# Kernel tuning notes

Hardware: AMD Instinct MI355X
Metric: run time of the kernel (lower is better)

Reference implementation:

```python
import jax, jax.numpy as jnp
import numpy as np

MOMENTUM = 0.99
EPS = 1e-5


def setup_inputs() -> dict:
    key = jax.random.key(0)
    k1, k2, k3, k4 = jax.random.split(key, 4)
    x = jax.random.normal(k1, (16, 256, 64, 64), dtype=jnp.float32)
    embed = jax.random.normal(k2, (2048, 256), dtype=jnp.float32)
    cluster_size = jax.random.uniform(k3, (2048,), dtype=jnp.float32)
    embed_avg = jax.random.normal(k4, (256, 2048), dtype=jnp.float32)
    return {"x": x, "embed": embed, "cluster_size": cluster_size, "embed_avg": embed_avg}


def reference(x, embed, cluster_size, embed_avg):
    # x: (b, c, h, w) with c == emb_dim; embed: (D, c)
    b, c, h, w = x.shape
    D = embed.shape[0]
    # flatten exactly as the torch code: transpose(1,-1) then reshape(-1, c)
    flat = jnp.swapaxes(x, 1, 3).reshape(-1, c)  # (N, c), N = b*w*h
    # L2 kNN with k=1, expressed as argmax of 2*q.k - |k|^2 - |q|^2 (as in _torch_knn)
    scores = (2.0 * (flat @ embed.T)
              - jnp.sum(embed * embed, axis=1)[None, :]
              - jnp.sum(flat * flat, axis=1, keepdims=True))  # (N, D)
    ids_flat = jnp.argmax(scores, axis=1)  # (N,)
    ids = ids_flat.reshape(b, h, w)
    # lookup + transpose(1,-1), mirroring the original op sequence
    quantized = jnp.swapaxes(embed[ids], 1, 3)  # (b, c, w, h) == (b, c, h, w) since h == w
    commit_loss = jnp.mean((x - quantized) ** 2)
    # EMA statistics (training branch). one-hot matmul expressed as segment sums (same math).
    onehot_sum = jax.ops.segment_sum(jnp.ones_like(ids_flat, dtype=flat.dtype), ids_flat,
                                     num_segments=D)  # (D,)
    embed_sum = jax.ops.segment_sum(flat, ids_flat, num_segments=D).T  # (c, D) == flat.T @ onehot
    new_cluster_size = MOMENTUM * cluster_size + (1.0 - MOMENTUM) * onehot_sum
    new_embed_avg = MOMENTUM * embed_avg + (1.0 - MOMENTUM) * embed_sum
    n = jnp.sum(new_cluster_size)
    cs_smoothed = n * (new_cluster_size + EPS) / (n + D * EPS)
    new_embed = new_embed_avg.T / cs_smoothed[:, None]  # (D, c)
    return quantized, commit_loss, ids, new_embed, new_cluster_size, new_embed_avg
```

## Files before the change

kernel.cpp:

```cpp
#include <hip/hip_runtime.h>

#define D_CODES 2048
#define C_DIM   256
#define MOM     0.99f
#define ONE_M   0.01f
#define EPSI    1e-5f
#define TAU     0.16f
#define RCAP    16384
#define SBCAP   2304

#define Q_OFF    0
#define LOSS_OFF 16777216
#define IDS_OFF  16777217
#define NE_OFF   16842753
#define NCS_OFF  17367041
#define NEA_OFF  17369089

#define WS_ICNT    0
#define WS_CNTF    2048
#define WS_OFFS    4096
#define WS_CURS    6144
#define WS_SUMX2   10240
#define WS_NTOT    11264
#define WS_RCNT    11268
#define WS_NSB     11269
#define WS_NORMS   11272
#define WS_RLIST   13320
#define WS_ESUM    29704
#define WS_E2      553992
#define WS_KEYH    816136
#define WS_M2H     1078280
#define WS_PLIST   1209352
#define WS_SBCODE  1274888
#define WS_SBSTART 1277192
#define WS_SBINFO  1279496
#define WS_LOSSP   1281800

typedef _Float16 half8 __attribute__((ext_vector_type(8)));
typedef __attribute__((ext_vector_type(4))) float f32x4;
typedef unsigned long long u64;

__device__ __forceinline__ f32x4 MFH(half8 a, half8 b, f32x4 c) {
    return __builtin_amdgcn_mfma_f32_16x16x32_f16(a, b, c, 0, 0, 0);
}
__device__ __forceinline__ unsigned enc_f(float v) {
    unsigned u = __float_as_uint(v);
    return (u & 0x80000000u) ? ~u : (u | 0x80000000u);
}
__device__ __forceinline__ float dec_f(unsigned u) {
    return (u & 0x80000000u) ? __uint_as_float(u & 0x7FFFFFFFu)
                             : __uint_as_float(~u);
}

__global__ __launch_bounds__(256) void k_init(
    const float* __restrict__ embed, const float* __restrict__ x,
    float* __restrict__ e2f, float* __restrict__ norms,
    float* __restrict__ esum, int* __restrict__ icnt,
    float* __restrict__ lossp, unsigned* __restrict__ rcnt,
    float* __restrict__ etg, float* __restrict__ xt,
    float* __restrict__ sumx2p)
{
    __shared__ float sh[8228];
    const int b = blockIdx.x, t = threadIdx.x;
    esum[(size_t)b * 256 + t] = 0.f;
    if (b < 64) {
        if (t < 32) sh[t] = 0.f;
        __syncthreads();
        char* e2 = (char*)e2f;
        const int s = b;
        #pragma unroll
        for (int it = 0; it < 4; ++it) {
            int u = it * 256 + t;
            int r = u >> 9, kc = (u >> 6) & 7, l = u & 63;
            int code = s * 32 + r * 16 + (l & 15);
            int ch0  = kc * 32 + ((l >> 4) << 3);
            const float* src = embed + (size_t)code * C_DIM + ch0;
            float4 v0 = *(const float4*)src;
            float4 v1 = *(const float4*)(src + 4);
            float vv[8] = {v0.x, v0.y, v0.z, v0.w, v1.x, v1.y, v1.z, v1.w};
            half8 hh;
            float p = 0.f;
            #pragma unroll
            for (int j = 0; j < 8; ++j) { hh[j] = (_Float16)vv[j]; p += vv[j] * vv[j]; }
            atomicAdd(&sh[r * 16 + (l & 15)], p);
            char* dst = e2 + (size_t)s * 16384 + (size_t)((r * 8 + kc) * 64 + l) * 16;
            *(half8*)dst = hh;
        }
        __syncthreads();
        if (t < 32) norms[s * 32 + t] = sh[t];
    } else if (b < 72) {
        icnt[(b - 64) * 256 + t] = 0;
    } else if (b < 81) {
        int j = (b - 72) * 256 + t;
        if (j < SBCAP) lossp[j] = 0.f;
    } else if (b == 81) {
        if (t == 0) *rcnt = 0u;
    } else if (b >= 128 && b < 384) {
        int code0 = (b - 128) * 8;
        #pragma unroll
        for (int j = 0; j < 8; ++j) {
            float v = embed[(size_t)(code0 + j) * C_DIM + t];
            etg[(size_t)t * D_CODES + code0 + j] = v;
        }
    } else if (b >= 384 && b < 1408) {
        float (*xs2)[257] = (float(*)[257])sh;
        float* wred = sh + 8224;
        const int xb = b - 384;
        const int bi = xb >> 6;
        const int hi = xb & 63;
        const int wl = t & 31;
        const int chh = t >> 5;
        float sx2 = 0.f;
        #pragma unroll
        for (int pass = 0; pass < 2; ++pass) {
            __syncthreads();
            #pragma unroll 8
            for (int k = 0; k < 32; ++k) {
                int ch = k * 8 + chh;
                float v = x[((size_t)(bi * C_DIM + ch)) * 4096 + hi * 64 + pass * 32 + wl];
                sx2 += v * v;
                xs2[wl][ch] = v;
            }
            __syncthreads();
            #pragma unroll 8
            for (int j = 0; j < 32; ++j) {
                int wi = pass * 32 + j;
                size_t n = (size_t)bi * 4096 + wi * 64 + hi;
                xt[n * C_DIM + t] = xs2[j][t];
            }
        }
        #pragma unroll
        for (int o = 32; o; o >>= 1) sx2 += __shfl_down(sx2, o);
        __syncthreads();
        if ((t & 63) == 0) wred[t >> 6] = sx2;
        __syncthreads();
        if (t == 0) sumx2p[xb] = wred[0] + wred[1] + wred[2] + wred[3];
    }
}

__global__ __launch_bounds__(256, 1) void k_main(
    const float* __restrict__ x, const float* __restrict__ e2f,
    const float* __restrict__ norms, u64* __restrict__ keyh,
    float* __restrict__ m2h)
{
    __shared__ char smem[33024];
    const int t  = threadIdx.x;
    const int l  = t & 63;
    const int w  = __builtin_amdgcn_readfirstlane(t >> 6);
    const int blk = blockIdx.x;
    const int h  = blk & 1;
    const int q  = (blk >> 1) & 15;
    const int bi = blk >> 5;
    const char* e2 = (const char*)e2f + (size_t)h * 32 * 16384 + (size_t)l * 16;

    half8 bx[4][8];
    {
        float* xs = (float*)smem;
        #pragma unroll
        for (int c = 0; c < 8; ++c) {
            __syncthreads();
            #pragma unroll
            for (int k = 0; k < 8; ++k) {
                int u = k * 256 + t;
                int wi0 = (u & 15) << 2;
                int hq  = (u >> 4) & 3;
                int chl = u >> 6;
                float4 v = *(const float4*)(x + ((size_t)(bi * C_DIM + c * 32 + chl)) * 4096
                                              + (4 * q + hq) * 64 + wi0);
                int pb = chl * 258 + hq * 64 + wi0;
                *(float2*)&xs[pb]     = make_float2(v.x, v.y);
                *(float2*)&xs[pb + 2] = make_float2(v.z, v.w);
            }
            __syncthreads();
            #pragma unroll
            for (int nt = 0; nt < 4; ++nt) {
                int px = w * 64 + nt * 16 + (l & 15);
                const int cb = (l >> 4) << 3;
                half8 hh;
                #pragma unroll
                for (int j = 0; j < 8; ++j)
                    hh[j] = (_Float16)xs[(cb + j) * 258 + px];
                bx[nt][c] = hh;
            }
        }
    }

    float m1[4] = {-3.4e38f, -3.4e38f, -3.4e38f, -3.4e38f};
    float m2[4] = {-3.4e38f, -3.4e38f, -3.4e38f, -3.4e38f};
    int   i1[4] = {0, 0, 0, 0};

    half8 ahA[8], ahB[8];
    auto loadbuf = [&](half8* buf, int ri) {
        const char* p = e2 + (size_t)ri * 8192;
        #pragma unroll
        for (int kc = 0; kc < 8; ++kc)
            buf[kc] = *(const half8*)(p + kc * 1024);
    };
    auto compute = [&](const half8* ah, int ri) {
        f32x4 z = {0.f, 0.f, 0.f, 0.f};
        f32x4 aA[4] = {z, z, z, z};
        #pragma unroll
        for (int kc = 0; kc < 8; ++kc) {
            #pragma unroll
            for (int nt = 0; nt < 4; ++nt)
                aA[nt] = MFH(ah[kc], bx[nt][kc], aA[nt]);
        }
        int c0 = h * 1024 + ri * 16 + ((l >> 4) << 2);
        float4 nrm = *(const float4*)(norms + c0);
        float nr[4] = {nrm.x, nrm.y, nrm.z, nrm.w};
        #pragma unroll
        for (int nt = 0; nt < 4; ++nt) {
            #pragma unroll
            for (int reg = 0; reg < 4; ++reg) {
                float sc = 2.f * aA[nt][reg] - nr[reg];
                int code = c0 + reg;
                if (sc > m1[nt]) { m2[nt] = m1[nt]; m1[nt] = sc; i1[nt] = code; }
                else             { m2[nt] = fmaxf(m2[nt], sc); }
            }
        }
    };

    loadbuf(ahA, 0);
    for (int ri = 0; ri < 64; ri += 2) {
        loadbuf(ahB, ri + 1);
        compute(ahA, ri);
        if (ri + 2 < 64) loadbuf(ahA, ri + 2);
        compute(ahB, ri + 1);
    }

    #pragma unroll
    for (int nt = 0; nt < 4; ++nt) {
        float a1 = m1[nt], a2 = m2[nt];
        int   ai = i1[nt];
        #pragma unroll
        for (int off = 16; off <= 32; off <<= 1) {
            float o1 = __shfl_xor(a1, off);
            int   oi = __shfl_xor(ai, off);
            float o2 = __shfl_xor(a2, off);
            if (o1 > a1)       { a2 = fmaxf(a1, o2); a1 = o1; ai = oi; }
            else if (o1 == a1) { if (oi < ai) ai = oi; a2 = a1; }
            else               { a2 = fmaxf(a2, o1); }
        }
        if (l < 16) {
            int wi = nt * 16 + l;
            int hi_ = 4 * q + w;
            int n = (bi << 12) + (wi << 6) + hi_;
            keyh[((size_t)h << 16) + n] = ((u64)enc_f(a1) << 32) | (unsigned)(~ai);
            m2h[(h << 16) + n] = a2;
        }
    }
}

__global__ __launch_bounds__(256) void k_merge(
    const u64* __restrict__ keyh, const float* __restrict__ m2h,
    float* __restrict__ out, int* __restrict__ icnt,
    unsigned* __restrict__ rcnt, int* __restrict__ rlist)
{
    int n = blockIdx.x * 256 + threadIdx.x;
    u64 kA = keyh[n], kB = keyh[65536 + n];
    float m2A = m2h[n], m2B = m2h[65536 + n];
    bool wA = kA >= kB;
    u64 kW = wA ? kA : kB, kL = wA ? kB : kA;
    float m2w = wA ? m2A : m2B;
    float sW = dec_f((unsigned)(kW >> 32));
    float sL = dec_f((unsigned)(kL >> 32));
    int code = (int)(~(unsigned)kW);
    out[IDS_OFF + n] = (float)code;
    atomicAdd(&icnt[code], 1);
    float gap = sW - fmaxf(m2w, sL);
    if (gap < TAU) {
        unsigned j = atomicAdd(rcnt, 1u);
        if (j < RCAP) rlist[j] = n;
    }
}

__global__ __launch_bounds__(256) void k_rescue(
    const float* __restrict__ xt, const float* __restrict__ etg,
    const float* __restrict__ norms, const unsigned* __restrict__ rcnt,
    const int* __restrict__ rlist, float* __restrict__ out,
    int* __restrict__ icnt)
{
    __shared__ float xs[8][257];
    __shared__ int nn[8];
    __shared__ u64 rk[4][8];
    const int t = threadIdx.x;
    const int l = t & 63;
    const int w = t >> 6;
    int nf = (int)min(*rcnt, (unsigned)RCAP);
    int nch = (nf + 7) >> 3;
    for (int chunk = blockIdx.x; chunk < nch; chunk += gridDim.x) {
        __syncthreads();
        if (t < 8) {
            int idx = chunk * 8 + t;
            nn[t] = rlist[idx < nf ? idx : (nf - 1)];
        }
        __syncthreads();
        #pragma unroll
        for (int p = 0; p < 8; ++p)
            xs[p][t] = xt[(size_t)nn[p] * C_DIM + t];
        __syncthreads();
        u64 bk[8];
        #pragma unroll
        for (int p = 0; p < 8; ++p) bk[p] = 0ull;
        #pragma unroll
        for (int rep = 0; rep < 2; ++rep) {
            const int d0 = rep * 1024 + t * 4;
            f32x4 acc[8];
            #pragma unroll
            for (int p = 0; p < 8; ++p) acc[p] = (f32x4){0.f, 0.f, 0.f, 0.f};
            for (int c = 0; c < C_DIM; ++c) {
                float4 e4 = *(const float4*)(etg + (size_t)c * D_CODES + d0);
                f32x4 ev = {e4.x, e4.y, e4.z, e4.w};
                #pragma unroll
                for (int p = 0; p < 8; ++p)
                    acc[p] += xs[p][c] * ev;
            }
            float4 nr = *(const float4*)(norms + d0);
            float nrr[4] = {nr.x, nr.y, nr.z, nr.w};
            #pragma unroll
            for (int p = 0; p < 8; ++p) {
                #pragma unroll
                for (int j = 0; j < 4; ++j) {
                    float sc = 2.f * acc[p][j] - nrr[j];
                    u64 key = ((u64)enc_f(sc) << 32) | (unsigned)(~(d0 + j));
                    if (key > bk[p]) bk[p] = key;
                }
            }
        }
        #pragma unroll
        for (int p = 0; p < 8; ++p) {
            u64 k0 = bk[p];
            #pragma unroll
            for (int o = 32; o; o >>= 1) {
                u64 ok = __shfl_down(k0, o);
                if (ok > k0) k0 = ok;
            }
            if (l == 0) rk[w][p] = k0;
        }
        __syncthreads();
        if (t < 8 && chunk * 8 + t < nf) {
            u64 k0 = rk[0][t];
            if (rk[1][t] > k0) k0 = rk[1][t];
            if (rk[2][t] > k0) k0 = rk[2][t];
            if (rk[3][t] > k0) k0 = rk[3][t];
            int n = nn[t];
            int newid = (int)(~(unsigned)k0);
            int old = (int)out[IDS_OFF + n];
            if (newid != old) {
                out[IDS_OFF + n] = (float)newid;
                atomicAdd(&icnt[old], -1);
                atomicAdd(&icnt[newid], 1);
            }
        }
    }
}

__global__ __launch_bounds__(256) void k_prefix(const int* __restrict__ icnt,
                                                const float* __restrict__ cs_in,
                                                int* __restrict__ offs,
                                                int* __restrict__ curs,
                                                float* __restrict__ cntf,
                                                int* __restrict__ sbcode,
                                                int* __restrict__ sbstart,
                                                int* __restrict__ sbinfo,
                                                int* __restrict__ nsbtot,
                                                float* __restrict__ ntot) {
    __shared__ int ps[256];
    __shared__ float fs[256];
    const int t = threadIdx.x;
    int c[8], o8[8];
    int s = 0;
    #pragma unroll
    for (int j = 0; j < 8; ++j) c[j] = icnt[t * 8 + j];
    #pragma unroll
    for (int j = 0; j < 8; ++j) { int tmp = c[j]; c[j] = s; s += tmp; }
    ps[t] = s;
    __syncthreads();
    for (int off = 1; off < 256; off <<= 1) {
        int v = (t >= off) ? ps[t - off] : 0;
        __syncthreads();
        ps[t] += v;
        __syncthreads();
    }
    int base = ps[t] - s;
    #pragma unroll
    for (int j = 0; j < 8; ++j) {
        int o = base + c[j];
        o8[j] = o;
        offs[t * 8 + j] = o;
        curs[t * 8 + j] = o;
        cntf[t * 8 + j] = (float)(icnt[t * 8 + j]);
    }
    int s2 = 0;
    int nb[8];
    #pragma unroll
    for (int j = 0; j < 8; ++j) {
        int cnt = icnt[t * 8 + j];
        nb[j] = (cnt + 255) >> 8;
        s2 += nb[j];
    }
    __syncthreads();
    ps[t] = s2;
    __syncthreads();
    for (int off = 1; off < 256; off <<= 1) {
        int v = (t >= off) ? ps[t - off] : 0;
        __syncthreads();
        ps[t] += v;
        __syncthreads();
    }
    int pos = ps[t] - s2;
    #pragma unroll
    for (int j = 0; j < 8; ++j) {
        int code = t * 8 + j;
        int cnt = icnt[code];
        int n = nb[j];
        for (int k = 0; k < n; ++k) {
            sbcode[pos]  = code;
            sbstart[pos] = o8[j] + k * 256;
            int len = cnt - k * 256; if (len > 256) len = 256;
            sbinfo[pos]  = len | ((n > 1) ? (1 << 16) : 0);
            ++pos;
        }
    }
    if (t == 255) *nsbtot = ps[255];
    float s3 = 0.f;
    #pragma unroll
    for (int j = 0; j < 8; ++j) s3 += cs_in[t * 8 + j];
    fs[t] = s3;
    __syncthreads();
    for (int o = 128; o; o >>= 1) { if (t < o) fs[t] += fs[t + o]; __syncthreads(); }
    if (t == 0) *ntot = MOM * fs[0] + ONE_M * 65536.0f;
}

__global__ __launch_bounds__(256) void k_scatter(const float* __restrict__ out,
                                                 int* __restrict__ curs,
                                                 int* __restrict__ plist) {
    int n = blockIdx.x * 256 + threadIdx.x;
    int id = (int)out[IDS_OFF + n];
    int pos = atomicAdd(&curs[id], 1);
    plist[pos] = n;
}

__global__ __launch_bounds__(256) void k_esum(
    const float* __restrict__ xt, const float* __restrict__ embed,
    const float* __restrict__ norms, const int* __restrict__ sbcode,
    const int* __restrict__ sbstart, const int* __restrict__ sbinfo,
    const int* __restrict__ plist, const int* __restrict__ nsbtot,
    float* __restrict__ esum, float* __restrict__ lossp)
{
    __shared__ int   ns[256];
    __shared__ float red[256];
    const int t = threadIdx.x;
    const int total = *nsbtot;
    for (int sb = blockIdx.x; sb < total; sb += gridDim.x) {
        const int d     = sbcode[sb];
        const int start = sbstart[sb];
        const int info  = sbinfo[sb];
        const int len   = info & 0xFFFF;
        const bool multi = (info >> 16) != 0;
        __syncthreads();
        if (t < len) ns[t] = plist[start + t];
        __syncthreads();
        float acc = 0.f;
        #pragma unroll 8
        for (int i = 0; i < len; ++i)
            acc += xt[(size_t)ns[i] * C_DIM + t];
        if (multi) atomicAdd(&esum[(size_t)t * D_CODES + d], acc);
        else       esum[(size_t)t * D_CODES + d] = acc;
        red[t] = acc * embed[(size_t)d * C_DIM + t];
        __syncthreads();
        for (int o = 128; o; o >>= 1) {
            if (t < o) red[t] += red[t + o];
            __syncthreads();
        }
        if (t == 0) lossp[sb] = 2.f * red[0] - (float)len * norms[d];
    }
}

__global__ __launch_bounds__(256) void k_quant(
    const float* __restrict__ embed, float* __restrict__ out)
{
    __shared__ int   ids_s[64];
    __shared__ float es[32][257];
    const int t  = threadIdx.x;
    const int bi = blockIdx.x >> 6;
    const int hi = blockIdx.x & 63;
    const int wl = t & 31;
    const int cg = t >> 5;
    if (t < 64) ids_s[t] = (int)out[IDS_OFF + ((size_t)bi << 12) + (t << 6) + hi];
    __syncthreads();
    #pragma unroll
    for (int pass = 0; pass < 2; ++pass) {
        #pragma unroll 8
        for (int p = 0; p < 32; ++p) {
            es[p][t] = embed[(size_t)ids_s[pass * 32 + p] * C_DIM + t];
        }
        __syncthreads();
        #pragma unroll 8
        for (int k = 0; k < 32; ++k) {
            int ch = k * 8 + cg;
            out[Q_OFF + ((size_t)(bi * C_DIM + ch)) * 4096 + hi * 64 + pass * 32 + wl]
                = es[wl][ch];
        }
        __syncthreads();
    }
}

__global__ __launch_bounds__(256) void k_final(
    const float* __restrict__ cs_in, const float* __restrict__ cntf,
    const float* __restrict__ embed_avg, const float* __restrict__ esum,
    const float* __restrict__ ntotp, const float* __restrict__ lossp,
    const float* __restrict__ sumx2p, float* __restrict__ out)
{
    const int b = blockIdx.x;
    const int t = threadIdx.x;
    if (b < 2048) {
        int ch = b >> 3;
        int d  = ((b & 7) << 8) + t;
        float ntot = *ntotp;
        float ncs  = MOM * cs_in[d] + ONE_M * cntf[d];
        if (b < 8) out[NCS_OFF + d] = ncs;
        float csm  = ntot * (ncs + EPSI) / (ntot + (float)D_CODES * EPSI);
        size_t i = (size_t)ch * D_CODES + d;
        float nea = MOM * embed_avg[i] + ONE_M * esum[i];
        out[NEA_OFF + i] = nea;
        out[NE_OFF + (size_t)d * C_DIM + ch] = nea / csm;
    } else {
        __shared__ float sm[256];
        float s1 = 0.f;
        for (int i = t; i < 1024; i += 256) s1 += sumx2p[i];
        float s2 = 0.f;
        for (int i = t; i < SBCAP; i += 256) s2 += lossp[i];
        sm[t] = s1 - s2;
        __syncthreads();
        for (int o = 128; o; o >>= 1) { if (t < o) sm[t] += sm[t + o]; __syncthreads(); }
        if (t == 0) out[LOSS_OFF] = sm[0] / 16777216.f;
    }
}

extern "C" void kernel_launch(void* const* d_in, const int* in_sizes, int n_in,
                              void* d_out, int out_size, void* d_ws, size_t ws_size,
                              hipStream_t stream) {
    const float* x     = (const float*)d_in[0];
    const float* embed = (const float*)d_in[1];
    const float* cs    = (const float*)d_in[2];
    const float* ea    = (const float*)d_in[3];
    float* out = (float*)d_out;
    float* ws  = (float*)d_ws;
    int*      icnt    = (int*)(ws + WS_ICNT);
    float*    cntf    = ws + WS_CNTF;
    int*      offs    = (int*)(ws + WS_OFFS);
    int*      curs    = (int*)(ws + WS_CURS);
    float*    sumx2p  = ws + WS_SUMX2;
    float*    ntot    = ws + WS_NTOT;
    unsigned* rcnt    = (unsigned*)(ws + WS_RCNT);
    int*      nsbtot  = (int*)(ws + WS_NSB);
    float*    norms   = ws + WS_NORMS;
    int*      rlist   = (int*)(ws + WS_RLIST);
    float*    esum    = ws + WS_ESUM;
    float*    e2      = ws + WS_E2;
    u64*      keyh    = (u64*)(ws + WS_KEYH);
    float*    m2h     = ws + WS_M2H;
    int*      plist   = (int*)(ws + WS_PLIST);
    int*      sbcode  = (int*)(ws + WS_SBCODE);
    int*      sbstart = (int*)(ws + WS_SBSTART);
    int*      sbinfo  = (int*)(ws + WS_SBINFO);
    float*    lossp   = ws + WS_LOSSP;
    float*    xt      = out + Q_OFF;
    float*    etg     = out + NEA_OFF;

    k_init<<<2048, 256, 0, stream>>>(embed, x, e2, norms, esum, icnt, lossp, rcnt,
                                     etg, xt, sumx2p);
    k_main<<<512, 256, 0, stream>>>(x, e2, norms, keyh, m2h);
    k_merge<<<256, 256, 0, stream>>>(keyh, m2h, out, icnt, rcnt, rlist);
    k_rescue<<<512, 256, 0, stream>>>(xt, etg, norms, rcnt, rlist, out, icnt);
    k_prefix<<<1, 256, 0, stream>>>(icnt, cs, offs, curs, cntf, sbcode, sbstart,
                                    sbinfo, nsbtot, ntot);
    k_scatter<<<256, 256, 0, stream>>>(out, curs, plist);
    k_esum<<<SBCAP, 256, 0, stream>>>(xt, embed, norms, sbcode, sbstart, sbinfo,
                                      plist, nsbtot, esum, lossp);
    k_quant<<<1024, 256, 0, stream>>>(embed, out);
    k_final<<<2049, 256, 0, stream>>>(cs, cntf, ea, esum, ntot, lossp, sumx2p, out);
}
```

Before: 296.9 us.

## Store transposed x as fp16, stage norms in LDS, fuse quant and final kernels

```diff
diff --git a/kernel.cpp b/kernel.cpp
--- a/kernel.cpp
+++ b/kernel.cpp
@@ -51,13 +51,16 @@
     return (u & 0x80000000u) ? __uint_as_float(u & 0x7FFFFFFFu)
                              : __uint_as_float(~u);
 }
+__device__ __forceinline__ unsigned short h_bits(_Float16 h) {
+    union { _Float16 f; unsigned short u; } c; c.f = h; return c.u;
+}
 
 __global__ __launch_bounds__(256) void k_init(
     const float* __restrict__ embed, const float* __restrict__ x,
     float* __restrict__ e2f, float* __restrict__ norms,
     float* __restrict__ esum, int* __restrict__ icnt,
     float* __restrict__ lossp, unsigned* __restrict__ rcnt,
-    float* __restrict__ etg, float* __restrict__ xt,
+    float* __restrict__ etg, unsigned short* __restrict__ xt2,
     float* __restrict__ sumx2p)
 {
     __shared__ float sh[8228];
@@ -122,11 +125,17 @@
                 xs2[wl][ch] = v;
             }
             __syncthreads();
-            #pragma unroll 8
-            for (int j = 0; j < 32; ++j) {
-                int wi = pass * 32 + j;
-                size_t n = (size_t)bi * 4096 + wi * 64 + hi;
-                xt[n * C_DIM + t] = xs2[j][t];
+            const int pxl = t >> 7;
+            const int ch2 = (t & 127) * 2;
+            #pragma unroll 4
+            for (int j2 = 0; j2 < 16; ++j2) {
+                int pl = j2 * 2 + pxl;
+                float v0 = xs2[pl][ch2];
+                float v1 = xs2[pl][ch2 + 1];
+                unsigned pack = ((unsigned)h_bits((_Float16)v1) << 16)
+                              | h_bits((_Float16)v0);
+                size_t n = (size_t)bi * 4096 + (size_t)(pass * 32 + pl) * 64 + hi;
+                *(unsigned*)(xt2 + n * C_DIM + ch2) = pack;
             }
         }
         #pragma unroll
@@ -183,7 +192,12 @@
                 bx[nt][c] = hh;
             }
         }
-    }
+        __syncthreads();
+        float* nlds = (float*)smem;
+        *(float4*)&nlds[t * 4] = *(const float4*)(norms + h * 1024 + t * 4);
+        __syncthreads();
+    }
+    const float* nlds = (const float*)smem;
 
     float m1[4] = {-3.4e38f, -3.4e38f, -3.4e38f, -3.4e38f};
     float m2[4] = {-3.4e38f, -3.4e38f, -3.4e38f, -3.4e38f};
@@ -197,6 +211,7 @@
             buf[kc] = *(const half8*)(p + kc * 1024);
     };
     auto compute = [&](const half8* ah, int ri) {
+        float4 nrm = *(const float4*)&nlds[ri * 16 + ((l >> 4) << 2)];
         f32x4 z = {0.f, 0.f, 0.f, 0.f};
         f32x4 aA[4] = {z, z, z, z};
         #pragma unroll
@@ -206,7 +221,6 @@
                 aA[nt] = MFH(ah[kc], bx[nt][kc], aA[nt]);
         }
         int c0 = h * 1024 + ri * 16 + ((l >> 4) << 2);
-        float4 nrm = *(const float4*)(norms + c0);
         float nr[4] = {nrm.x, nrm.y, nrm.z, nrm.w};
         #pragma unroll
         for (int nt = 0; nt < 4; ++nt) {
@@ -275,7 +289,7 @@
 }
 
 __global__ __launch_bounds__(256) void k_rescue(
-    const float* __restrict__ xt, const float* __restrict__ etg,
+    const float* __restrict__ x, const float* __restrict__ etg,
     const float* __restrict__ norms, const unsigned* __restrict__ rcnt,
     const int* __restrict__ rlist, float* __restrict__ out,
     int* __restrict__ icnt)
@@ -296,8 +310,11 @@
         }
         __syncthreads();
         #pragma unroll
-        for (int p = 0; p < 8; ++p)
-            xs[p][t] = xt[(size_t)nn[p] * C_DIM + t];
+        for (int p = 0; p < 8; ++p) {
+            int n = nn[p];
+            int bi = n >> 12, wi = (n >> 6) & 63, hi = n & 63;
+            xs[p][t] = x[((size_t)(bi * C_DIM + t)) * 4096 + hi * 64 + wi];
+        }
         __syncthreads();
         u64 bk[8];
         #pragma unroll
@@ -442,7 +459,7 @@
 }
 
 __global__ __launch_bounds__(256) void k_esum(
-    const float* __restrict__ xt, const float* __restrict__ embed,
+    const unsigned short* __restrict__ xt2, const float* __restrict__ embed,
     const float* __restrict__ norms, const int* __restrict__ sbcode,
     const int* __restrict__ sbstart, const int* __restrict__ sbinfo,
     const int* __restrict__ plist, const int* __restrict__ nsbtot,
@@ -450,6 +467,7 @@
 {
     __shared__ int   ns[256];
     __shared__ float red[256];
+    const _Float16* xth = (const _Float16*)xt2;
     const int t = threadIdx.x;
     const int total = *nsbtot;
     for (int sb = blockIdx.x; sb < total; sb += gridDim.x) {
@@ -464,7 +482,7 @@
         float acc = 0.f;
         #pragma unroll 8
         for (int i = 0; i < len; ++i)
-            acc += xt[(size_t)ns[i] * C_DIM + t];
+            acc += (float)xth[(size_t)ns[i] * C_DIM + t];
         if (multi) atomicAdd(&esum[(size_t)t * D_CODES + d], acc);
         else       esum[(size_t)t * D_CODES + d] = acc;
         red[t] = acc * embed[(size_t)d * C_DIM + t];
@@ -477,56 +495,54 @@
     }
 }
 
-__global__ __launch_bounds__(256) void k_quant(
-    const float* __restrict__ embed, float* __restrict__ out)
+__global__ __launch_bounds__(256) void k_post(
+    const float* __restrict__ embed, const float* __restrict__ cs_in,
+    const float* __restrict__ cntf, const float* __restrict__ embed_avg,
+    const float* __restrict__ esum, const float* __restrict__ ntotp,
+    const float* __restrict__ lossp, const float* __restrict__ sumx2p,
+    float* __restrict__ out)
 {
-    __shared__ int   ids_s[64];
-    __shared__ float es[32][257];
-    const int t  = threadIdx.x;
-    const int bi = blockIdx.x >> 6;
-    const int hi = blockIdx.x & 63;
-    const int wl = t & 31;
-    const int cg = t >> 5;
-    if (t < 64) ids_s[t] = (int)out[IDS_OFF + ((size_t)bi << 12) + (t << 6) + hi];
-    __syncthreads();
-    #pragma unroll
-    for (int pass = 0; pass < 2; ++pass) {
-        #pragma unroll 8
-        for (int p = 0; p < 32; ++p) {
-            es[p][t] = embed[(size_t)ids_s[pass * 32 + p] * C_DIM + t];
-        }
-        __syncthreads();
-        #pragma unroll 8
-        for (int k = 0; k < 32; ++k) {
-            int ch = k * 8 + cg;
-            out[Q_OFF + ((size_t)(bi * C_DIM + ch)) * 4096 + hi * 64 + pass * 32 + wl]
-                = es[wl][ch];
-        }
-        __syncthreads();
-    }
-}
-
-__global__ __launch_bounds__(256) void k_final(
-    const float* __restrict__ cs_in, const float* __restrict__ cntf,
-    const float* __restrict__ embed_avg, const float* __restrict__ esum,
-    const float* __restrict__ ntotp, const float* __restrict__ lossp,
-    const float* __restrict__ sumx2p, float* __restrict__ out)
-{
+    __shared__ float shm[8456];
     const int b = blockIdx.x;
     const int t = threadIdx.x;
-    if (b < 2048) {
-        int ch = b >> 3;
-        int d  = ((b & 7) << 8) + t;
+    if (b < 1024) {
+        int* ids_s = (int*)shm;
+        float (*es)[257] = (float(*)[257])(shm + 64);
+        const int bi = b >> 6;
+        const int hi = b & 63;
+        const int wl = t & 31;
+        const int cg = t >> 5;
+        if (t < 64) ids_s[t] = (int)out[IDS_OFF + ((size_t)bi << 12) + (t << 6) + hi];
+        __syncthreads();
+        #pragma unroll
+        for (int pass = 0; pass < 2; ++pass) {
+            #pragma unroll 8
+            for (int p = 0; p < 32; ++p) {
+                es[p][t] = embed[(size_t)ids_s[pass * 32 + p] * C_DIM + t];
+            }
+            __syncthreads();
+            #pragma unroll 8
+            for (int k = 0; k < 32; ++k) {
+                int ch = k * 8 + cg;
+                out[Q_OFF + ((size_t)(bi * C_DIM + ch)) * 4096 + hi * 64 + pass * 32 + wl]
+                    = es[wl][ch];
+            }
+            __syncthreads();
+        }
+    } else if (b < 3072) {
+        int bb = b - 1024;
+        int ch = bb >> 3;
+        int d  = ((bb & 7) << 8) + t;
         float ntot = *ntotp;
         float ncs  = MOM * cs_in[d] + ONE_M * cntf[d];
-        if (b < 8) out[NCS_OFF + d] = ncs;
+        if (bb < 8) out[NCS_OFF + d] = ncs;
         float csm  = ntot * (ncs + EPSI) / (ntot + (float)D_CODES * EPSI);
         size_t i = (size_t)ch * D_CODES + d;
         float nea = MOM * embed_avg[i] + ONE_M * esum[i];
         out[NEA_OFF + i] = nea;
         out[NE_OFF + (size_t)d * C_DIM + ch] = nea / csm;
     } else {
-        __shared__ float sm[256];
+        float* sm = shm;
         float s1 = 0.f;
         for (int i = t; i < 1024; i += 256) s1 += sumx2p[i];
         float s2 = 0.f;
@@ -566,19 +582,19 @@
     int*      sbstart = (int*)(ws + WS_SBSTART);
     int*      sbinfo  = (int*)(ws + WS_SBINFO);
     float*    lossp   = ws + WS_LOSSP;
-    float*    xt      = out + Q_OFF;
+    unsigned short* xt2 = (unsigned short*)(out + Q_OFF);
     float*    etg     = out + NEA_OFF;
 
     k_init<<<2048, 256, 0, stream>>>(embed, x, e2, norms, esum, icnt, lossp, rcnt,
-                                     etg, xt, sumx2p);
+                                     etg, xt2, sumx2p);
     k_main<<<512, 256, 0, stream>>>(x, e2, norms, keyh, m2h);
     k_merge<<<256, 256, 0, stream>>>(keyh, m2h, out, icnt, rcnt, rlist);
-    k_rescue<<<512, 256, 0, stream>>>(xt, etg, norms, rcnt, rlist, out, icnt);
+    k_rescue<<<512, 256, 0, stream>>>(x, etg, norms, rcnt, rlist, out, icnt);
     k_prefix<<<1, 256, 0, stream>>>(icnt, cs, offs, curs, cntf, sbcode, sbstart,
                                     sbinfo, nsbtot, ntot);
     k_scatter<<<256, 256, 0, stream>>>(out, curs, plist);
-    k_esum<<<SBCAP, 256, 0, stream>>>(xt, embed, norms, sbcode, sbstart, sbinfo,
+    k_esum<<<SBCAP, 256, 0, stream>>>(xt2, embed, norms, sbcode, sbstart, sbinfo,
                                       plist, nsbtot, esum, lossp);
-    k_quant<<<1024, 256, 0, stream>>>(embed, out);
-    k_final<<<2049, 256, 0, stream>>>(cs, cntf, ea, esum, ntot, lossp, sumx2p, out);
-}
+    k_post<<<3073, 256, 0, stream>>>(embed, cs, cntf, ea, esum, ntot, lossp,
+                                     sumx2p, out);
+}
```

Measured after the change: 285.5 us. 1.04x faster.
